# Kernel tuning notes

Measured on AMD Instinct MI355X. Metric: run time of the kernel, lower is better.

Reference implementation:

```python
import jax, jax.numpy as jnp
import numpy as np

B, S, E, H = 8, 1024, 768, 12
D = E // H  # per-head dim


def setup_inputs() -> dict:
    key = jax.random.key(0)
    ks = jax.random.split(key, 9)
    glorot = lambda k: jax.random.normal(k, (E, E), jnp.float32) * np.sqrt(2.0 / (E + E))
    return {
        "inputs": jax.random.normal(ks[0], (B, S, E), jnp.float32),
        "Wq": glorot(ks[1]), "bq": jnp.zeros((E,), jnp.float32),
        "Wk": glorot(ks[2]), "bk": jnp.zeros((E,), jnp.float32),
        "Wv": glorot(ks[3]), "bv": jnp.zeros((E,), jnp.float32),
        "Wo": glorot(ks[4]), "bo": jnp.zeros((E,), jnp.float32),
    }


def reference(inputs, Wq, bq, Wk, bk, Wv, bv, Wo, bo):
    b, s, e = inputs.shape
    # QKV projections then split heads: [B,S,E] -> [B,H,S,D]
    def heads(x):
        return x.reshape(b, s, H, D).transpose(0, 2, 1, 3)
    q = heads(inputs @ Wq + bq)
    k = heads(inputs @ Wk + bk)
    v = heads(inputs @ Wv + bv)
    scale = 1.0 / jnp.sqrt(jnp.asarray(D, inputs.dtype))
    scores = jnp.einsum("bhqd,bhkd->bhqk", q, k) * scale
    weights = jax.nn.softmax(scores, axis=-1)  # attn_drop rate 0 -> identity
    attn = jnp.einsum("bhqk,bhkd->bhqd", weights, v)
    concat = attn.transpose(0, 2, 1, 3).reshape(b, s, e)
    out = concat @ Wo + bo  # proj_drop rate 0 -> identity
    return out
```

## Files before the change

### kernel.cpp

```cpp
#include <hip/hip_runtime.h>
#include <math.h>

#define BB 8
#define SS 1024
#define EE 768
#define HH 12
#define DD 64
#define MM (BB*SS)

typedef __attribute__((ext_vector_type(8))) short short8;
typedef __attribute__((ext_vector_type(4))) short short4v;
typedef __attribute__((ext_vector_type(4))) float f32x4;

static __device__ __forceinline__ short f2bf(float x) {
    unsigned u = __float_as_uint(x);
    u += 0x7fffu + ((u >> 16) & 1u);
    return (short)(u >> 16);
}
static __device__ __forceinline__ short f2bf_fast(float x) {
    return (short)((__float_as_uint(x) + 0x8000u) >> 16);
}

static __device__ __forceinline__ void gload_lds16(const void* g, void* l) {
    __builtin_amdgcn_global_load_lds((__attribute__((address_space(1))) void*)g,
                                     (__attribute__((address_space(3))) void*)l,
                                     16, 0, 0);
}

__global__ __launch_bounds__(256)
void cast_x(const float* __restrict__ src, short* __restrict__ dst) {
    const long i = ((long)blockIdx.x * 256 + threadIdx.x) * 4;
    float4 v = *(const float4*)&src[i];
    short4v o;
    o.x = f2bf(v.x); o.y = f2bf(v.y); o.z = f2bf(v.z); o.w = f2bf(v.w);
    *(short4v*)&dst[i] = o;
}

__global__ __launch_bounds__(256)
void wcast_t(const float* __restrict__ W0, const float* __restrict__ W1,
             const float* __restrict__ W2, const float* __restrict__ W3,
             short* __restrict__ Wt) {
    __shared__ short T[64][72];
    const int z = blockIdx.z;
    const float* sp = (z == 0) ? W0 : (z == 1) ? W1 : (z == 2) ? W2 : W3;
    short* dp = Wt + (long)z * EE * EE;
    const int i0 = blockIdx.y * 64;
    const int j0 = blockIdx.x * 64;
    const int tid = threadIdx.x;
#pragma unroll
    for (int rep = 0; rep < 4; ++rep) {
        const int r = (tid >> 4) + rep * 16;
        const int c = (tid & 15) * 4;
        float4 v = *(const float4*)&sp[(long)(i0 + r) * EE + j0 + c];
        T[c + 0][r] = f2bf(v.x);
        T[c + 1][r] = f2bf(v.y);
        T[c + 2][r] = f2bf(v.z);
        T[c + 3][r] = f2bf(v.w);
    }
    __syncthreads();
#pragma unroll
    for (int rep = 0; rep < 4; ++rep) {
        const int rr = (tid >> 4) + rep * 16;
        const int cc = (tid & 15) * 4;
        short4v o;
        o.x = T[rr][cc + 0]; o.y = T[rr][cc + 1];
        o.z = T[rr][cc + 2]; o.w = T[rr][cc + 3];
        *(short4v*)&dp[(long)(j0 + rr) * EE + i0 + cc] = o;
    }
}

#define GEMM_CORE(Abase, Bbase, row0, col0)                                     \
    f32x4 acc[4][4];                                                            \
    _Pragma("unroll") for (int i = 0; i < 4; ++i)                               \
        _Pragma("unroll") for (int j = 0; j < 4; ++j)                           \
            acc[i][j] = (f32x4){0.f, 0.f, 0.f, 0.f};                            \
    const int rm = (w & 1) * 64, cn = (w >> 1) * 64;                            \
    for (int k0 = 0; k0 < EE; k0 += 64) {                                       \
        __syncthreads();                                                        \
        _Pragma("unroll") for (int i = 0; i < 4; ++i) {                         \
            const int chunk = w * 256 + i * 64 + lane;                          \
            const int r = chunk >> 3;                                           \
            const int cs = (((chunk & 7) ^ (r & 7)) << 3);                      \
            short* ldsA = Al + (w * 256 + i * 64) * 8;                          \
            short* ldsB = Bl + (w * 256 + i * 64) * 8;                          \
            gload_lds16(&Abase[(long)(row0 + r) * EE + k0 + cs], ldsA);         \
            gload_lds16(&Bbase[(long)(col0 + r) * EE + k0 + cs], ldsB);         \
        }                                                                       \
        __syncthreads();                                                        \
        _Pragma("unroll") for (int ks = 0; ks < 2; ++ks) {                      \
            short8 af[4], bf[4];                                                \
            _Pragma("unroll") for (int t = 0; t < 4; ++t)                       \
                af[t] = *(const short8*)&Al[(rm + t * 16 + m) * 64 +            \
                                            (((ks * 4 + quad) ^ (m & 7)) << 3)]; \
            _Pragma("unroll") for (int t = 0; t < 4; ++t)                       \
                bf[t] = *(const short8*)&Bl[(cn + t * 16 + m) * 64 +            \
                                            (((ks * 4 + quad) ^ (m & 7)) << 3)]; \
            _Pragma("unroll") for (int mt = 0; mt < 4; ++mt)                    \
                _Pragma("unroll") for (int nt = 0; nt < 4; ++nt)                \
                    acc[mt][nt] = __builtin_amdgcn_mfma_f32_16x16x32_bf16(      \
                        af[mt], bf[nt], acc[mt][nt], 0, 0, 0);                  \
        }                                                                       \
    }

#define TSTRIDE 134

#define QSCALE 0.1803368801111204f

__global__ __launch_bounds__(256)
void gemm_qkv(const short* __restrict__ Xb, const short* __restrict__ Wt,
              const float* __restrict__ bq, const float* __restrict__ bk,
              const float* __restrict__ bv,
              short* __restrict__ Qb, short* __restrict__ Kb,
              short* __restrict__ Vb) {
    __shared__ short SMEM[128 * TSTRIDE];
    short* const Al = SMEM;
    short* const Bl = SMEM + 128 * 64;
    const int tid = threadIdx.x, w = tid >> 6, lane = tid & 63;
    const int m = lane & 15, quad = lane >> 4;
    const int wsel = blockIdx.x / 6;
    const int colt = blockIdx.x % 6;
    const int row0 = blockIdx.y * 128;
    const int col0 = colt * 128;
    const short* Wsel = Wt + (long)wsel * EE * EE;
    const float* bias = (wsel == 0) ? bq : (wsel == 1) ? bk : bv;

    GEMM_CORE(Xb, Wsel, row0, col0)

    __syncthreads();
    const int b = row0 >> 10, s0 = row0 & 1023;

    if (wsel < 2) {
        const float scale = (wsel == 0) ? QSCALE : 1.0f;
        short* QK = (wsel == 0) ? Qb : Kb;
#pragma unroll
        for (int nt = 0; nt < 4; ++nt) {
            const float bvv = bias[col0 + cn + nt * 16 + m];
#pragma unroll
            for (int mt = 0; mt < 4; ++mt)
#pragma unroll
                for (int r = 0; r < 4; ++r)
                    SMEM[(rm + mt * 16 + quad * 4 + r) * TSTRIDE + cn + nt * 16 + m] =
                        f2bf((acc[mt][nt][r] + bvv) * scale);
        }
        __syncthreads();
#pragma unroll
        for (int rep = 0; rep < 8; ++rep) {
            const int chunk = tid + rep * 256;
            const int row = chunk >> 4;
            const int cc = (chunk & 15) * 8;
            const int colg = col0 + cc;
            const int h = colg >> 6, d = colg & 63;
            short8 v = *(const short8*)&SMEM[row * TSTRIDE + cc];
            *(short8*)&QK[((long)(b * HH + h) * SS + s0 + row) * DD + d] = v;
        }
    } else {
#pragma unroll
        for (int nt = 0; nt < 4; ++nt) {
            const float bvv = bias[col0 + cn + nt * 16 + m];
#pragma unroll
            for (int mt = 0; mt < 4; ++mt) {
                const int rowb = rm + mt * 16 + quad * 4;
                short4v o;
                o.x = f2bf(acc[mt][nt][0] + bvv);
                o.y = f2bf(acc[mt][nt][1] + bvv);
                o.z = f2bf(acc[mt][nt][2] + bvv);
                o.w = f2bf(acc[mt][nt][3] + bvv);
                *(short4v*)&SMEM[(cn + nt * 16 + m) * TSTRIDE + rowb] = o;
            }
        }
        __syncthreads();
#pragma unroll
        for (int rep = 0; rep < 8; ++rep) {
            const int chunk = tid + rep * 256;
            const int col = chunk >> 4;
            const int sc8 = (chunk & 15) * 8;
            const int colg = col0 + col;
            const int h = colg >> 6, d = colg & 63;
            short8 v = *(const short8*)&SMEM[col * TSTRIDE + sc8];
            *(short8*)&Vb[((long)(b * HH + h) * DD + d) * SS + s0 + sc8] = v;
        }
    }
}

__global__ __launch_bounds__(256)
void gemm_proj(const short* __restrict__ Cb, const short* __restrict__ WoT,
               const float* __restrict__ bo, float* __restrict__ out) {
    __shared__ short Al[128 * 64];
    __shared__ short Bl[128 * 64];
    const int tid = threadIdx.x, w = tid >> 6, lane = tid & 63;
    const int m = lane & 15, quad = lane >> 4;
    const int row0 = blockIdx.y * 128;
    const int col0 = blockIdx.x * 128;

    GEMM_CORE(Cb, WoT, row0, col0)

#pragma unroll
    for (int nt = 0; nt < 4; ++nt) {
        const int colg = col0 + cn + nt * 16 + m;
        const float bvv = bo[colg];
#pragma unroll
        for (int mt = 0; mt < 4; ++mt)
#pragma unroll
            for (int r = 0; r < 4; ++r) {
                const int srow = row0 + rm + mt * 16 + quad * 4 + r;
                out[(long)srow * EE + colg] = acc[mt][nt][r] + bvv;
            }
    }
}

__global__ __launch_bounds__(256)
void attn_mfma(const short* __restrict__ Q,
               const short* __restrict__ K,
               const short* __restrict__ Vt,
               short* __restrict__ out) {
    __shared__ short Kl[64 * 72];
    __shared__ short Vl[64 * 72];
    __shared__ short Pl[4 * 32 * 72];

    const int tid  = threadIdx.x;
    const int w    = tid >> 6;
    const int l    = tid & 63;
    const int m    = l & 15;
    const int quad = l >> 4;
    const int h = blockIdx.y, b = blockIdx.z;
    const int q0 = blockIdx.x * 128;
    const long bh = (long)(b * HH + h);

    const short* Qg = Q  + bh * SS * DD;
    const short* Kg = K  + bh * SS * DD;
    const short* Vg = Vt + bh * DD * SS;

    short8 aq[2][2];
#pragma unroll
    for (int g = 0; g < 2; ++g) {
        const int row = q0 + w * 32 + g * 16 + m;
        aq[g][0] = *(const short8*)(Qg + (long)row * DD + quad * 8);
        aq[g][1] = *(const short8*)(Qg + (long)row * DD + 32 + quad * 8);
    }

    short8 ones;
#pragma unroll
    for (int i = 0; i < 8; ++i) ones[i] = (short)0x3F80;

    f32x4 O[2][4], lacc[2];
#pragma unroll
    for (int g = 0; g < 2; ++g) {
        lacc[g] = (f32x4){0.f, 0.f, 0.f, 0.f};
#pragma unroll
        for (int dt = 0; dt < 4; ++dt) O[g][dt] = (f32x4){0.f, 0.f, 0.f, 0.f};
    }

    for (int kt = 0; kt < 16; ++kt) {
        const int k0 = kt * 64;
        __syncthreads();
#pragma unroll
        for (int rep = 0; rep < 2; ++rep) {
            const int seg = tid + rep * 256;
            const int r = seg >> 3, s = seg & 7;
            *(short8*)(Kl + r * 72 + s * 8) =
                *(const short8*)(Kg + (long)(k0 + r) * DD + s * 8);
            *(short8*)(Vl + r * 72 + s * 8) =
                *(const short8*)(Vg + (long)r * SS + k0 + s * 8);
        }
        __syncthreads();

        f32x4 sc[2][4];
#pragma unroll
        for (int nt = 0; nt < 4; ++nt) {
            const short* kb = Kl + (nt * 16 + m) * 72 + quad * 8;
            short8 b0 = *(const short8*)kb;
            short8 b1 = *(const short8*)(kb + 32);
#pragma unroll
            for (int g = 0; g < 2; ++g) {
                f32x4 a = (f32x4){0.f, 0.f, 0.f, 0.f};
                a = __builtin_amdgcn_mfma_f32_16x16x32_bf16(aq[g][0], b0, a, 0, 0, 0);
                a = __builtin_amdgcn_mfma_f32_16x16x32_bf16(aq[g][1], b1, a, 0, 0, 0);
                sc[g][nt] = a;
            }
        }

#pragma unroll
        for (int g = 0; g < 2; ++g)
#pragma unroll
            for (int nt = 0; nt < 4; ++nt)
#pragma unroll
                for (int r = 0; r < 4; ++r)
                    sc[g][nt][r] = __builtin_amdgcn_exp2f(sc[g][nt][r]);

        short* Pw = Pl + w * 32 * 72;
#pragma unroll
        for (int g = 0; g < 2; ++g)
#pragma unroll
            for (int nt = 0; nt < 4; ++nt)
#pragma unroll
                for (int r = 0; r < 4; ++r)
                    Pw[(g * 16 + quad * 4 + r) * 72 + nt * 16 + m] =
                        f2bf_fast(sc[g][nt][r]);

        short8 ap[2][2];
#pragma unroll
        for (int g = 0; g < 2; ++g) {
            ap[g][0] = *(const short8*)(Pw + (g * 16 + m) * 72 + quad * 8);
            ap[g][1] = *(const short8*)(Pw + (g * 16 + m) * 72 + 32 + quad * 8);
        }

#pragma unroll
        for (int g = 0; g < 2; ++g) {
            lacc[g] = __builtin_amdgcn_mfma_f32_16x16x32_bf16(ap[g][0], ones, lacc[g], 0, 0, 0);
            lacc[g] = __builtin_amdgcn_mfma_f32_16x16x32_bf16(ap[g][1], ones, lacc[g], 0, 0, 0);
        }
#pragma unroll
        for (int dt = 0; dt < 4; ++dt) {
            const short* vb = Vl + (dt * 16 + m) * 72 + quad * 8;
            short8 b0 = *(const short8*)vb;
            short8 b1 = *(const short8*)(vb + 32);
#pragma unroll
            for (int g = 0; g < 2; ++g) {
                O[g][dt] = __builtin_amdgcn_mfma_f32_16x16x32_bf16(ap[g][0], b0, O[g][dt], 0, 0, 0);
                O[g][dt] = __builtin_amdgcn_mfma_f32_16x16x32_bf16(ap[g][1], b1, O[g][dt], 0, 0, 0);
            }
        }
    }

#pragma unroll
    for (int g = 0; g < 2; ++g)
#pragma unroll
        for (int r = 0; r < 4; ++r) {
            const float inv = 1.0f / lacc[g][r];
            const int qo = q0 + w * 32 + g * 16 + quad * 4 + r;
            short* orow = out + ((long)(b * SS + qo)) * EE + h * DD;
#pragma unroll
            for (int dt = 0; dt < 4; ++dt)
                orow[dt * 16 + m] = f2bf(O[g][dt][r] * inv);
        }
}

extern "C" void kernel_launch(void* const* d_in, const int* in_sizes, int n_in,
                              void* d_out, int out_size, void* d_ws, size_t ws_size,
                              hipStream_t stream) {
    const float* X  = (const float*)d_in[0];
    const float* Wq = (const float*)d_in[1];
    const float* bq = (const float*)d_in[2];
    const float* Wk = (const float*)d_in[3];
    const float* bk = (const float*)d_in[4];
    const float* Wv = (const float*)d_in[5];
    const float* bv = (const float*)d_in[6];
    const float* Wo = (const float*)d_in[7];
    const float* bo = (const float*)d_in[8];

    const long SEG = (long)BB * HH * SS * DD;
    const long WSEG = (long)EE * EE;
    short* Xb = (short*)d_ws;
    short* Wt = Xb + SEG;
    short* Qb = Wt + 4 * WSEG;
    short* Kb = Qb + SEG;
    short* Vb = Kb + SEG;
    short* Cb = Vb + SEG;

    cast_x<<<dim3(MM * EE / 4 / 256), 256, 0, stream>>>(X, Xb);
    wcast_t<<<dim3(12, 12, 4), 256, 0, stream>>>(Wq, Wk, Wv, Wo, Wt);

    gemm_qkv<<<dim3(18, 64), 256, 0, stream>>>(Xb, Wt, bq, bk, bv, Qb, Kb, Vb);

    attn_mfma<<<dim3(SS / 128, HH, BB), 256, 0, stream>>>(Qb, Kb, Vb, Cb);

    gemm_proj<<<dim3(6, 64), 256, 0, stream>>>(Cb, Wt + 3 * WSEG, bo,
                                               (float*)d_out);
}
```

Baseline: 215.7 us.

## Double-buffer attention K/V via async LDS loads and remap blocks per XCD

The attention kernel now keeps two K/V LDS buffers filled with direct global-to-LDS loads into an XOR-swizzled layout. It prefetches the next 64-key tile while computing on the current one, and raises wave priority around the MFMA sections. All three kernels remap block indices so that blocks sharing rows or heads land on the same XCD, aiming for better L2 reuse. This costs more LDS per block for attention, which may lower occupancy.

```diff
diff --git a/kernel.cpp b/kernel.cpp
--- a/kernel.cpp
+++ b/kernel.cpp
@@ -117,9 +117,15 @@
     short* const Bl = SMEM + 128 * 64;
     const int tid = threadIdx.x, w = tid >> 6, lane = tid & 63;
     const int m = lane & 15, quad = lane >> 4;
-    const int wsel = blockIdx.x / 6;
-    const int colt = blockIdx.x % 6;
-    const int row0 = blockIdx.y * 128;
+
+    const int flat = blockIdx.x + 18 * blockIdx.y;
+    const int id   = (flat & 7) * 144 + (flat >> 3);
+    const int xcd  = id / 144;
+    const int lcl  = id % 144;
+    const int colw = lcl >> 3;
+    const int wsel = colw / 6;
+    const int colt = colw % 6;
+    const int row0 = (xcd * 8 + (lcl & 7)) * 128;
     const int col0 = colt * 128;
     const short* Wsel = Wt + (long)wsel * EE * EE;
     const float* bias = (wsel == 0) ? bq : (wsel == 1) ? bk : bv;
@@ -189,8 +195,13 @@
     __shared__ short Bl[128 * 64];
     const int tid = threadIdx.x, w = tid >> 6, lane = tid & 63;
     const int m = lane & 15, quad = lane >> 4;
-    const int row0 = blockIdx.y * 128;
-    const int col0 = blockIdx.x * 128;
+
+    const int flat = blockIdx.x + 6 * blockIdx.y;
+    const int id   = (flat & 7) * 48 + (flat >> 3);
+    const int xcd  = id / 48;
+    const int lcl  = id % 48;
+    const int row0 = (xcd * 8 + (lcl & 7)) * 128;
+    const int col0 = (lcl >> 3) * 128;
 
     GEMM_CORE(Cb, WoT, row0, col0)
 
@@ -208,13 +219,77 @@
     }
 }
 
+
+#define ATTN_STAGE(Kdst, Vdst, k0)                                            \
+    do {                                                                      \
+        _Pragma("unroll") for (int i = 0; i < 2; ++i) {                       \
+            const int chunk = w * 128 + i * 64 + l;                           \
+            const int r = chunk >> 3;                                         \
+            const int cs = ((chunk & 7) ^ (r & 7)) << 3;                      \
+            gload_lds16(&Kg[(long)((k0) + r) * DD + cs],                      \
+                        (Kdst) + (w * 128 + i * 64) * 8);                     \
+            gload_lds16(&Vg[(long)r * SS + (k0) + cs],                        \
+                        (Vdst) + (w * 128 + i * 64) * 8);                     \
+        }                                                                     \
+    } while (0)
+
+#define ATTN_COMPUTE(Kbuf, Vbuf)                                              \
+    do {                                                                      \
+        f32x4 sc[2][4];                                                       \
+        __builtin_amdgcn_s_setprio(1);                                        \
+        _Pragma("unroll") for (int nt = 0; nt < 4; ++nt) {                    \
+            const short* kb = (Kbuf) + (nt * 16 + m) * 64;                    \
+            short8 b0 = *(const short8*)&kb[(quad ^ (m & 7)) << 3];           \
+            short8 b1 = *(const short8*)&kb[((4 + quad) ^ (m & 7)) << 3];     \
+            _Pragma("unroll") for (int g = 0; g < 2; ++g) {                   \
+                f32x4 a = (f32x4){0.f, 0.f, 0.f, 0.f};                        \
+                a = __builtin_amdgcn_mfma_f32_16x16x32_bf16(aq[g][0], b0, a, 0, 0, 0); \
+                a = __builtin_amdgcn_mfma_f32_16x16x32_bf16(aq[g][1], b1, a, 0, 0, 0); \
+                sc[g][nt] = a;                                                \
+            }                                                                 \
+        }                                                                     \
+        __builtin_amdgcn_s_setprio(0);                                        \
+        _Pragma("unroll") for (int g = 0; g < 2; ++g)                         \
+            _Pragma("unroll") for (int nt = 0; nt < 4; ++nt)                  \
+                _Pragma("unroll") for (int r = 0; r < 4; ++r)                 \
+                    sc[g][nt][r] = __builtin_amdgcn_exp2f(sc[g][nt][r]);      \
+        short* Pw = Pl + w * 32 * 72;                                         \
+        _Pragma("unroll") for (int g = 0; g < 2; ++g)                         \
+            _Pragma("unroll") for (int nt = 0; nt < 4; ++nt)                  \
+                _Pragma("unroll") for (int r = 0; r < 4; ++r)                 \
+                    Pw[(g * 16 + quad * 4 + r) * 72 + nt * 16 + m] =          \
+                        f2bf_fast(sc[g][nt][r]);                              \
+        short8 ap[2][2];                                                      \
+        _Pragma("unroll") for (int g = 0; g < 2; ++g) {                       \
+            ap[g][0] = *(const short8*)(Pw + (g * 16 + m) * 72 + quad * 8);   \
+            ap[g][1] = *(const short8*)(Pw + (g * 16 + m) * 72 + 32 + quad * 8); \
+        }                                                                     \
+        __builtin_amdgcn_s_setprio(1);                                        \
+        _Pragma("unroll") for (int g = 0; g < 2; ++g) {                       \
+            lacc[g] = __builtin_amdgcn_mfma_f32_16x16x32_bf16(ap[g][0], ones, lacc[g], 0, 0, 0); \
+            lacc[g] = __builtin_amdgcn_mfma_f32_16x16x32_bf16(ap[g][1], ones, lacc[g], 0, 0, 0); \
+        }                                                                     \
+        _Pragma("unroll") for (int dt = 0; dt < 4; ++dt) {                    \
+            const short* vb = (Vbuf) + (dt * 16 + m) * 64;                    \
+            short8 b0 = *(const short8*)&vb[(quad ^ (m & 7)) << 3];           \
+            short8 b1 = *(const short8*)&vb[((4 + quad) ^ (m & 7)) << 3];     \
+            _Pragma("unroll") for (int g = 0; g < 2; ++g) {                   \
+                O[g][dt] = __builtin_amdgcn_mfma_f32_16x16x32_bf16(ap[g][0], b0, O[g][dt], 0, 0, 0); \
+                O[g][dt] = __builtin_amdgcn_mfma_f32_16x16x32_bf16(ap[g][1], b1, O[g][dt], 0, 0, 0); \
+            }                                                                 \
+        }                                                                     \
+        __builtin_amdgcn_s_setprio(0);                                        \
+    } while (0)
+
 __global__ __launch_bounds__(256)
 void attn_mfma(const short* __restrict__ Q,
                const short* __restrict__ K,
                const short* __restrict__ Vt,
                short* __restrict__ out) {
-    __shared__ short Kl[64 * 72];
-    __shared__ short Vl[64 * 72];
+    __shared__ short K0l[64 * 64];
+    __shared__ short K1l[64 * 64];
+    __shared__ short V0l[64 * 64];
+    __shared__ short V1l[64 * 64];
     __shared__ short Pl[4 * 32 * 72];
 
     const int tid  = threadIdx.x;
@@ -222,13 +297,18 @@
     const int l    = tid & 63;
     const int m    = l & 15;
     const int quad = l >> 4;
-    const int h = blockIdx.y, b = blockIdx.z;
-    const int q0 = blockIdx.x * 128;
-    const long bh = (long)(b * HH + h);
-
-    const short* Qg = Q  + bh * SS * DD;
-    const short* Kg = K  + bh * SS * DD;
-    const short* Vg = Vt + bh * DD * SS;
+
+    const int flat = blockIdx.x + 8 * blockIdx.y + 96 * blockIdx.z;
+    const int id   = (flat & 7) * 96 + (flat >> 3);
+    const int qt   = id & 7;
+    const int bh   = id >> 3;
+    const int b    = bh / HH;
+    const int h    = bh % HH;
+    const int q0   = qt * 128;
+
+    const short* Qg = Q  + (long)bh * SS * DD;
+    const short* Kg = K  + (long)bh * SS * DD;
+    const short* Vg = Vt + (long)bh * DD * SS;
 
     short8 aq[2][2];
 #pragma unroll
@@ -250,76 +330,18 @@
         for (int dt = 0; dt < 4; ++dt) O[g][dt] = (f32x4){0.f, 0.f, 0.f, 0.f};
     }
 
-    for (int kt = 0; kt < 16; ++kt) {
-        const int k0 = kt * 64;
+    ATTN_STAGE(K0l, V0l, 0);
+    __syncthreads();
+
+#pragma unroll 1
+    for (int kt2 = 0; kt2 < 8; ++kt2) {
+        const int k0 = kt2 * 128;
+        ATTN_STAGE(K1l, V1l, k0 + 64);
+        ATTN_COMPUTE(K0l, V0l);
         __syncthreads();
-#pragma unroll
-        for (int rep = 0; rep < 2; ++rep) {
-            const int seg = tid + rep * 256;
-            const int r = seg >> 3, s = seg & 7;
-            *(short8*)(Kl + r * 72 + s * 8) =
-                *(const short8*)(Kg + (long)(k0 + r) * DD + s * 8);
-            *(short8*)(Vl + r * 72 + s * 8) =
-                *(const short8*)(Vg + (long)r * SS + k0 + s * 8);
-        }
+        if (kt2 < 7) ATTN_STAGE(K0l, V0l, k0 + 128);
+        ATTN_COMPUTE(K1l, V1l);
         __syncthreads();
-
-        f32x4 sc[2][4];
-#pragma unroll
-        for (int nt = 0; nt < 4; ++nt) {
-            const short* kb = Kl + (nt * 16 + m) * 72 + quad * 8;
-            short8 b0 = *(const short8*)kb;
-            short8 b1 = *(const short8*)(kb + 32);
-#pragma unroll
-            for (int g = 0; g < 2; ++g) {
-                f32x4 a = (f32x4){0.f, 0.f, 0.f, 0.f};
-                a = __builtin_amdgcn_mfma_f32_16x16x32_bf16(aq[g][0], b0, a, 0, 0, 0);
-                a = __builtin_amdgcn_mfma_f32_16x16x32_bf16(aq[g][1], b1, a, 0, 0, 0);
-                sc[g][nt] = a;
-            }
-        }
-
-#pragma unroll
-        for (int g = 0; g < 2; ++g)
-#pragma unroll
-            for (int nt = 0; nt < 4; ++nt)
-#pragma unroll
-                for (int r = 0; r < 4; ++r)
-                    sc[g][nt][r] = __builtin_amdgcn_exp2f(sc[g][nt][r]);
-
-        short* Pw = Pl + w * 32 * 72;
-#pragma unroll
-        for (int g = 0; g < 2; ++g)
-#pragma unroll
-            for (int nt = 0; nt < 4; ++nt)
-#pragma unroll
-                for (int r = 0; r < 4; ++r)
-                    Pw[(g * 16 + quad * 4 + r) * 72 + nt * 16 + m] =
-                        f2bf_fast(sc[g][nt][r]);
-
-        short8 ap[2][2];
-#pragma unroll
-        for (int g = 0; g < 2; ++g) {
-            ap[g][0] = *(const short8*)(Pw + (g * 16 + m) * 72 + quad * 8);
-            ap[g][1] = *(const short8*)(Pw + (g * 16 + m) * 72 + 32 + quad * 8);
-        }
-
-#pragma unroll
-        for (int g = 0; g < 2; ++g) {
-            lacc[g] = __builtin_amdgcn_mfma_f32_16x16x32_bf16(ap[g][0], ones, lacc[g], 0, 0, 0);
-            lacc[g] = __builtin_amdgcn_mfma_f32_16x16x32_bf16(ap[g][1], ones, lacc[g], 0, 0, 0);
-        }
-#pragma unroll
-        for (int dt = 0; dt < 4; ++dt) {
-            const short* vb = Vl + (dt * 16 + m) * 72 + quad * 8;
-            short8 b0 = *(const short8*)vb;
-            short8 b1 = *(const short8*)(vb + 32);
-#pragma unroll
-            for (int g = 0; g < 2; ++g) {
-                O[g][dt] = __builtin_amdgcn_mfma_f32_16x16x32_bf16(ap[g][0], b0, O[g][dt], 0, 0, 0);
-                O[g][dt] = __builtin_amdgcn_mfma_f32_16x16x32_bf16(ap[g][1], b1, O[g][dt], 0, 0, 0);
-            }
-        }
     }
 
 #pragma unroll
```

Measured after the change: 206.7 us. -4.2%, faster.
